# Optimization experiments

Hardware: AMD Instinct MI355X
Metric: run time of the kernel (lower is better)

Reference implementation:

```python
import jax, jax.numpy as jnp
import numpy as np

N = 4_194_304          # number of rays
DAMPING = 0.5          # LM(0.5)
MAX_DELTA = 1000.0     # clamp on LM step
N_ITER = 30            # no_grad warmup iterations
XMIN, XMAX, TAU = -1.0, 1.0, 1.0


def _surface_F(pts, c):
    # implicit parabolic rod: F(p) = x - c*(y^2 + z^2); pts: [N,3]
    return pts[..., 0] - c * (pts[..., 1] ** 2 + pts[..., 2] ** 2)


def _lm_delta(P, V, t, c):
    # Levenberg-Marquardt step for f(t) = F(P + t*V):
    # delta = f * f' / (f'^2 + damping), clamped to [-max_delta, max_delta]
    pts = P + t[:, None] * V                     # [N,3]
    f = _surface_F(pts, c)                       # [N]
    # f'(t) = gradF(pts) . V, gradF = (1, -2c*y, -2c*z)
    fp = V[:, 0] - 2.0 * c * (pts[:, 1] * V[:, 1] + pts[:, 2] * V[:, 2])
    delta = f * fp / (fp * fp + DAMPING)
    return jnp.clip(delta, -MAX_DELTA, MAX_DELTA)


def setup_inputs() -> dict:
    key = jax.random.key(0)
    k1, k2 = jax.random.split(key, 2)
    P = jax.random.normal(k1, (N, 3), jnp.float32) * 2.0
    V = jax.random.normal(k2, (N, 3), jnp.float32)
    V = V / jnp.linalg.norm(V, axis=-1, keepdims=True)
    a, b = 0.3, -0.2
    Rz = jnp.array([[np.cos(a), -np.sin(a), 0.0],
                    [np.sin(a),  np.cos(a), 0.0],
                    [0.0,        0.0,       1.0]], jnp.float32)
    Ry = jnp.array([[np.cos(b), 0.0, np.sin(b)],
                    [0.0,       1.0, 0.0],
                    [-np.sin(b), 0.0, np.cos(b)]], jnp.float32)
    R = Rz @ Ry                                  # rigid rotation [3,3]
    T = jnp.array([0.1, -0.2, 0.05], jnp.float32)
    c = jnp.float32(0.05)
    loss_in = jnp.float32(0.0)
    return {"P": P, "V": V, "R": R, "T": T, "c": c, "loss_in": loss_in}


def reference(P, V, R, T, c, loss_in):
    n = P.shape[0]
    # transform.inverse_points / inverse_vectors: R^T (p - T), R^T v
    P_local = (P - T) @ R                        # [N,3]
    V_local = V @ R                              # [N,3]

    # 30 no-grad LM iterations (torch.no_grad -> stop_gradient on inputs)
    Pl = jax.lax.stop_gradient(P_local)
    Vl = jax.lax.stop_gradient(V_local)
    cs = jax.lax.stop_gradient(c)

    def body(i, t):
        return t - _lm_delta(Pl, Vl, t, cs)

    t0 = jax.lax.fori_loop(0, N_ITER, body, jnp.zeros((n,), jnp.float32))

    # final differentiable LM step
    t = t0 - _lm_delta(P_local, V_local, t0, c)

    points_local = P_local + t[:, None] * V_local
    scale = jnp.mean(jnp.abs(jnp.array([XMIN, XMAX, TAU], jnp.float32)))
    F = _surface_F(points_local, c) / scale
    loss = loss_in + jnp.sum(F ** 2) / n
    return loss
```

## Files before the change

kernel.cpp:

```cpp
#include <hip/hip_runtime.h>


#define LM_ITERS 31
constexpr float DAMPING = 0.5f;

__global__ __launch_bounds__(256) void rod_kernel(
    const float* __restrict__ P, const float* __restrict__ V,
    const float* __restrict__ Rm, const float* __restrict__ Tv,
    const float* __restrict__ c_ptr, double* __restrict__ ws, int n)
{
    const float c  = c_ptr[0];
    const float r00 = Rm[0], r01 = Rm[1], r02 = Rm[2];
    const float r10 = Rm[3], r11 = Rm[4], r12 = Rm[5];
    const float r20 = Rm[6], r21 = Rm[7], r22 = Rm[8];
    const float t0 = Tv[0], t1 = Tv[1], t2 = Tv[2];

    const int tid      = blockIdx.x * blockDim.x + threadIdx.x;
    const int nthreads = gridDim.x * blockDim.x;

    const float4* P4 = (const float4*)P;
    const float4* V4 = (const float4*)V;

    double acc = 0.0;

    float nA[4], f[4], fp[4];
    auto setup4 = [&](const float4& qa, const float4& qb, const float4& qc,
                      const float4& ua, const float4& ub, const float4& uc) {
        const float px[4] = {qa.x, qa.w, qb.z, qc.y};
        const float py[4] = {qa.y, qb.x, qb.w, qc.z};
        const float pz[4] = {qa.z, qb.y, qc.x, qc.w};
        const float wx[4] = {ua.x, ua.w, ub.z, uc.y};
        const float wy[4] = {ua.y, ub.x, ub.w, uc.z};
        const float wz[4] = {ua.z, ub.y, uc.x, uc.w};
        #pragma unroll
        for (int r = 0; r < 4; ++r) {
            const float qx = px[r] - t0, qy = py[r] - t1, qz = pz[r] - t2;
            const float plx = qx * r00 + qy * r10 + qz * r20;
            const float ply = qx * r01 + qy * r11 + qz * r21;
            const float plz = qx * r02 + qy * r12 + qz * r22;
            const float vlx = wx[r] * r00 + wy[r] * r10 + wz[r] * r20;
            const float vly = wx[r] * r01 + wy[r] * r11 + wz[r] * r21;
            const float vlz = wx[r] * r02 + wy[r] * r12 + wz[r] * r22;
            nA[r] = c * (vly * vly + vlz * vlz);
            f[r]  = plx - c * (ply * ply + plz * plz);
            fp[r] = vlx - 2.0f * c * (ply * vly + plz * vlz);
        }
    };

    auto iterate = [&]() {
        #pragma unroll 1
        for (int it = 0; it < LM_ITERS; ++it) {
            #pragma unroll
            for (int r = 0; r < 4; ++r) {
                const float den = fmaf(fp[r], fp[r], DAMPING);
                const float rcp = __builtin_amdgcn_rcpf(den);
                const float d   = (f[r] * fp[r]) * rcp;
                const float tmp = fmaf(nA[r], d, fp[r]);
                f[r]  = fmaf(-d, tmp, f[r]);
                fp[r] = fmaf(nA[r], d, tmp);
            }
        }
    };

    auto accum = [&](int g) {
        #pragma unroll
        for (int r = 0; r < 4; ++r)
            if (4 * g + r < n) acc += (double)f[r] * (double)f[r];
    };

    const int g0 = tid;
    const int g1 = tid + nthreads;
    const int g2 = tid + 2 * nthreads;
    const int g3 = tid + 3 * nthreads;

    float4 a0{}, b0{}, c0{}, u0{}, v0{}, w0{};
    if (4 * g0 < n) {
        a0 = P4[g0 * 3 + 0]; b0 = P4[g0 * 3 + 1]; c0 = P4[g0 * 3 + 2];
        u0 = V4[g0 * 3 + 0]; v0 = V4[g0 * 3 + 1]; w0 = V4[g0 * 3 + 2];
    }
    setup4(a0, b0, c0, u0, v0, w0);

    float4 a1{}, b1{}, c1{}, u1{}, v1{}, w1{};
    if (4 * g1 < n) {
        a1 = P4[g1 * 3 + 0]; b1 = P4[g1 * 3 + 1]; c1 = P4[g1 * 3 + 2];
        u1 = V4[g1 * 3 + 0]; v1 = V4[g1 * 3 + 1]; w1 = V4[g1 * 3 + 2];
    }
    iterate();
    accum(g0);

    setup4(a1, b1, c1, u1, v1, w1);
    float4 a2{}, b2{}, c2{}, u2{}, v2{}, w2{};
    if (4 * g2 < n) {
        a2 = P4[g2 * 3 + 0]; b2 = P4[g2 * 3 + 1]; c2 = P4[g2 * 3 + 2];
        u2 = V4[g2 * 3 + 0]; v2 = V4[g2 * 3 + 1]; w2 = V4[g2 * 3 + 2];
    }
    iterate();
    accum(g1);

    setup4(a2, b2, c2, u2, v2, w2);
    float4 a3{}, b3{}, c3{}, u3{}, v3{}, w3{};
    if (4 * g3 < n) {
        a3 = P4[g3 * 3 + 0]; b3 = P4[g3 * 3 + 1]; c3 = P4[g3 * 3 + 2];
        u3 = V4[g3 * 3 + 0]; v3 = V4[g3 * 3 + 1]; w3 = V4[g3 * 3 + 2];
    }
    iterate();
    accum(g2);

    setup4(a3, b3, c3, u3, v3, w3);
    iterate();
    accum(g3);

    for (int off = 32; off > 0; off >>= 1)
        acc += __shfl_down(acc, off, 64);
    __shared__ double sacc[4];
    const int lane = threadIdx.x & 63, wave = threadIdx.x >> 6;
    if (lane == 0) sacc[wave] = acc;
    __syncthreads();
    if (threadIdx.x == 0) {
        atomicAdd(ws, sacc[0] + sacc[1] + sacc[2] + sacc[3]);
    }
}

__global__ void rod_finalize(const double* __restrict__ ws,
                             const float* __restrict__ loss_in,
                             float* __restrict__ out, double inv_n)
{
    out[0] = (float)(ws[0] * inv_n + (double)loss_in[0]);
}

extern "C" void kernel_launch(void* const* d_in, const int* in_sizes, int n_in,
                              void* d_out, int out_size, void* d_ws, size_t ws_size,
                              hipStream_t stream) {
    const float* P       = (const float*)d_in[0];
    const float* V       = (const float*)d_in[1];
    const float* R       = (const float*)d_in[2];
    const float* T       = (const float*)d_in[3];
    const float* c       = (const float*)d_in[4];
    const float* loss_in = (const float*)d_in[5];

    const int n = in_sizes[0] / 3;

    hipMemsetAsync(d_ws, 0, sizeof(double), stream);

    const int threads = (n + 15) / 16;
    const int block   = 256;
    const int grid    = (threads + block - 1) / block;
    rod_kernel<<<grid, block, 0, stream>>>(P, V, R, T, c, (double*)d_ws, n);
    rod_finalize<<<1, 1, 0, stream>>>((const double*)d_ws, loss_in,
                                      (float*)d_out, 1.0 / (double)n);
}
```

Measured before the change: 134.3 us.

## Use packed float2 math in LM loop and halve rays per thread

The per-ray LM iteration now uses two-wide vector types, so the fma and multiply work can map to packed FP32 instructions (v_pk_fma_f32) on CDNA. The reciprocal stays scalar. Each thread now handles two groups of four rays instead of four, so the grid is twice as large and there are more waves to hide latency. The trade-off is less software pipelining per thread, more blocks and more atomics, and the compiler may not actually emit packed instructions.

Measured after the change: 144.3 us. +7.4%, slower.

```diff
diff --git a/kernel.cpp b/kernel.cpp
--- a/kernel.cpp
+++ b/kernel.cpp
@@ -3,6 +3,8 @@
 
 #define LM_ITERS 31
 constexpr float DAMPING = 0.5f;
+
+typedef float v2f __attribute__((ext_vector_type(2)));
 
 __global__ __launch_bounds__(256) void rod_kernel(
     const float* __restrict__ P, const float* __restrict__ V,
@@ -17,13 +19,16 @@
 
     const int tid      = blockIdx.x * blockDim.x + threadIdx.x;
     const int nthreads = gridDim.x * blockDim.x;
+    const int g0 = tid;
+    const int g1 = tid + nthreads;
 
     const float4* P4 = (const float4*)P;
     const float4* V4 = (const float4*)V;
 
     double acc = 0.0;
 
-    float nA[4], f[4], fp[4];
+    v2f nA0, nA1, f0, f1, fp0, fp1;
+
     auto setup4 = [&](const float4& qa, const float4& qb, const float4& qc,
                       const float4& ua, const float4& ub, const float4& uc) {
         const float px[4] = {qa.x, qa.w, qb.z, qc.y};
@@ -41,37 +46,51 @@
             const float vlx = wx[r] * r00 + wy[r] * r10 + wz[r] * r20;
             const float vly = wx[r] * r01 + wy[r] * r11 + wz[r] * r21;
             const float vlz = wx[r] * r02 + wy[r] * r12 + wz[r] * r22;
-            nA[r] = c * (vly * vly + vlz * vlz);
-            f[r]  = plx - c * (ply * ply + plz * plz);
-            fp[r] = vlx - 2.0f * c * (ply * vly + plz * vlz);
+            const float na = c * (vly * vly + vlz * vlz);
+            const float fv = plx - c * (ply * ply + plz * plz);
+            const float fq = vlx - 2.0f * c * (ply * vly + plz * vlz);
+            if (r < 2) { nA0[r & 1] = na; f0[r & 1] = fv; fp0[r & 1] = fq; }
+            else       { nA1[r & 1] = na; f1[r & 1] = fv; fp1[r & 1] = fq; }
         }
     };
 
+    const v2f vdamp = {DAMPING, DAMPING};
     auto iterate = [&]() {
         #pragma unroll 1
         for (int it = 0; it < LM_ITERS; ++it) {
-            #pragma unroll
-            for (int r = 0; r < 4; ++r) {
-                const float den = fmaf(fp[r], fp[r], DAMPING);
-                const float rcp = __builtin_amdgcn_rcpf(den);
-                const float d   = (f[r] * fp[r]) * rcp;
-                const float tmp = fmaf(nA[r], d, fp[r]);
-                f[r]  = fmaf(-d, tmp, f[r]);
-                fp[r] = fmaf(nA[r], d, tmp);
+            {
+                const v2f den = __builtin_elementwise_fma(fp0, fp0, vdamp);
+                v2f rcp;
+                rcp.x = __builtin_amdgcn_rcpf(den.x);
+                rcp.y = __builtin_amdgcn_rcpf(den.y);
+                const v2f d   = (f0 * fp0) * rcp;
+                const v2f tmp = __builtin_elementwise_fma(nA0, d, fp0);
+                f0  = __builtin_elementwise_fma(-d, tmp, f0);
+                fp0 = __builtin_elementwise_fma(nA0, d, tmp);
+            }
+            {
+                const v2f den = __builtin_elementwise_fma(fp1, fp1, vdamp);
+                v2f rcp;
+                rcp.x = __builtin_amdgcn_rcpf(den.x);
+                rcp.y = __builtin_amdgcn_rcpf(den.y);
+                const v2f d   = (f1 * fp1) * rcp;
+                const v2f tmp = __builtin_elementwise_fma(nA1, d, fp1);
+                f1  = __builtin_elementwise_fma(-d, tmp, f1);
+                fp1 = __builtin_elementwise_fma(nA1, d, tmp);
             }
         }
     };
 
     auto accum = [&](int g) {
-        #pragma unroll
-        for (int r = 0; r < 4; ++r)
-            if (4 * g + r < n) acc += (double)f[r] * (double)f[r];
+        if (4 * g + 4 <= n) {
+            acc += (double)f0.x * (double)f0.x + (double)f0.y * (double)f0.y;
+            acc += (double)f1.x * (double)f1.x + (double)f1.y * (double)f1.y;
+        } else {
+            const float fs[4] = {f0.x, f0.y, f1.x, f1.y};
+            for (int r = 0; r < 4; ++r)
+                if (4 * g + r < n) acc += (double)fs[r] * (double)fs[r];
+        }
     };
-
-    const int g0 = tid;
-    const int g1 = tid + nthreads;
-    const int g2 = tid + 2 * nthreads;
-    const int g3 = tid + 3 * nthreads;
 
     float4 a0{}, b0{}, c0{}, u0{}, v0{}, w0{};
     if (4 * g0 < n) {
@@ -81,34 +100,18 @@
     setup4(a0, b0, c0, u0, v0, w0);
 
     float4 a1{}, b1{}, c1{}, u1{}, v1{}, w1{};
-    if (4 * g1 < n) {
+    const bool has1 = (4 * g1 < n);
+    if (has1) {
         a1 = P4[g1 * 3 + 0]; b1 = P4[g1 * 3 + 1]; c1 = P4[g1 * 3 + 2];
         u1 = V4[g1 * 3 + 0]; v1 = V4[g1 * 3 + 1]; w1 = V4[g1 * 3 + 2];
     }
+
     iterate();
-    accum(g0);
+    if (4 * g0 < n) accum(g0);
 
     setup4(a1, b1, c1, u1, v1, w1);
-    float4 a2{}, b2{}, c2{}, u2{}, v2{}, w2{};
-    if (4 * g2 < n) {
-        a2 = P4[g2 * 3 + 0]; b2 = P4[g2 * 3 + 1]; c2 = P4[g2 * 3 + 2];
-        u2 = V4[g2 * 3 + 0]; v2 = V4[g2 * 3 + 1]; w2 = V4[g2 * 3 + 2];
-    }
     iterate();
-    accum(g1);
-
-    setup4(a2, b2, c2, u2, v2, w2);
-    float4 a3{}, b3{}, c3{}, u3{}, v3{}, w3{};
-    if (4 * g3 < n) {
-        a3 = P4[g3 * 3 + 0]; b3 = P4[g3 * 3 + 1]; c3 = P4[g3 * 3 + 2];
-        u3 = V4[g3 * 3 + 0]; v3 = V4[g3 * 3 + 1]; w3 = V4[g3 * 3 + 2];
-    }
-    iterate();
-    accum(g2);
-
-    setup4(a3, b3, c3, u3, v3, w3);
-    iterate();
-    accum(g3);
+    if (has1) accum(g1);
 
     for (int off = 32; off > 0; off >>= 1)
         acc += __shfl_down(acc, off, 64);
@@ -142,7 +145,7 @@
 
     hipMemsetAsync(d_ws, 0, sizeof(double), stream);
 
-    const int threads = (n + 15) / 16;
+    const int threads = (n + 7) / 8;
     const int block   = 256;
     const int grid    = (threads + block - 1) / block;
     rod_kernel<<<grid, block, 0, stream>>>(P, V, R, T, c, (double*)d_ws, n);
```
